# Optimization experiments

Hardware: AMD Instinct MI355X
Metric: run time of the kernel (lower is better)

The kernel has to match this reference:

```python
import jax, jax.numpy as jnp
import numpy as np

N_NODES = 50000
N_EDGES = 800000
EMBED_DIM = 256
HIDDEN_DIM = 128
OUT_DIM = 12
N_TARGETS = 4096


def gcn_conv(x, edge_index, W, b):
    """PyG-style GCNConv: add self-loops, symmetric deg^-1/2 normalization,
    linear transform then sparse aggregation."""
    n = x.shape[0]
    loop = jnp.arange(n)
    src = jnp.concatenate([edge_index[0], loop])
    dst = jnp.concatenate([edge_index[1], loop])
    # degree of destination nodes (incl. self loops)
    deg = jax.ops.segment_sum(jnp.ones_like(dst, dtype=x.dtype), dst, num_segments=n)
    dinv = jnp.where(deg > 0, jax.lax.rsqrt(deg), 0.0)
    norm = dinv[src] * dinv[dst]                     # [E+n]
    h = x @ W                                        # [n, out] transform first (PyG order)
    msgs = h[src] * norm[:, None]                    # [E+n, out]
    return jax.ops.segment_sum(msgs, dst, num_segments=n) + b


def setup_inputs() -> dict:
    key = jax.random.key(0)
    ks = jax.random.split(key, 9)
    x = jax.random.normal(ks[0], (N_NODES, EMBED_DIM), dtype=jnp.float32)
    edge_index = jax.random.randint(ks[1], (2, N_EDGES), 0, N_NODES, dtype=jnp.int64)
    target_mask = jax.random.randint(ks[2], (N_TARGETS,), 0, N_NODES, dtype=jnp.int64)
    s1 = 1.0 / np.sqrt(EMBED_DIM)
    s2 = 1.0 / np.sqrt(HIDDEN_DIM)
    W1 = jax.random.uniform(ks[3], (EMBED_DIM, HIDDEN_DIM), jnp.float32, -s1, s1)
    b1 = jnp.zeros((HIDDEN_DIM,), jnp.float32)
    W2 = jax.random.uniform(ks[4], (HIDDEN_DIM, HIDDEN_DIM), jnp.float32, -s2, s2)
    b2 = jnp.zeros((HIDDEN_DIM,), jnp.float32)
    Wr = jax.random.uniform(ks[5], (HIDDEN_DIM, OUT_DIM), jnp.float32, -s2, s2)
    br = jax.random.uniform(ks[6], (OUT_DIM,), jnp.float32, -s2, s2)
    return {"x": x, "edge_index": edge_index, "target_mask": target_mask,
            "W1": W1, "b1": b1, "W2": W2, "b2": b2, "Wr": Wr, "br": br}


def reference(x, edge_index, target_mask, W1, b1, W2, b2, Wr, br):
    h = jax.nn.relu(gcn_conv(x, edge_index, W1, b1))
    h = jax.nn.relu(gcn_conv(h, edge_index, W2, b2))
    pred = h[target_mask] @ Wr + br                  # [N_TARGETS, OUT_DIM]
    return pred
```

## Files before the change

### kernel.cpp

```cpp
#include <hip/hip_runtime.h>
#include <math.h>

#define N_NODES 50000
#define N_EDGES 800000
#define EMBED 256
#define HID 128
#define OUTD 12
#define N_TGT 4096

#define SCAN_NB 196
#define NPART 8
#define NODES_PER_PART 6250
#define RCAP 64
#define NB_G1 782

typedef short bf16x8 __attribute__((ext_vector_type(8)));
typedef float f32x4 __attribute__((ext_vector_type(4)));
typedef int intx4 __attribute__((ext_vector_type(4)));

__device__ __forceinline__ unsigned short f2b(float f) {
    union { float f; unsigned int u; } v;
    v.f = f;
    unsigned int u = v.u;
    return (unsigned short)((u + 0x7FFFu + ((u >> 16) & 1u)) >> 16);
}

__device__ __forceinline__ float b2f(unsigned short s) {
    union { unsigned int u; float f; } v;
    v.u = ((unsigned int)s) << 16;
    return v.f;
}

__global__ __launch_bounds__(256) void k_prelude(int* __restrict__ counts,
                                                 const float* __restrict__ W1,
                                                 unsigned short* __restrict__ Wt1,
                                                 const float* __restrict__ W2,
                                                 unsigned short* __restrict__ Wt2) {
    int i = blockIdx.x * 256 + threadIdx.x;
    if (i < N_NODES) counts[i] = 0;
    if (i < 32768) {
        int nn = i >> 8, k = i & 255;
        Wt1[nn * 256 + k] = f2b(W1[(size_t)k * 128 + nn]);
    } else if (i < 49152) {
        int j = i - 32768;
        int nn = j >> 7, k = j & 127;
        Wt2[nn * 128 + k] = f2b(W2[(size_t)k * 128 + nn]);
    }
}

template <int K, bool IS_BF16>
__device__ __forceinline__ void gemm_body(int gb, int tid, const void* __restrict__ Xv,
                                          const unsigned short* __restrict__ Wt,
                                          unsigned short* __restrict__ Hb, int n,
                                          unsigned short* As ) {
    const int row0 = gb * 64;
    const int w = tid >> 6, lane = tid & 63;
    const int lr = lane & 15, lg = lane >> 4;
    constexpr int NKS = K / 32;

    bf16x8 bfr[NKS][2];
#pragma unroll
    for (int ks = 0; ks < NKS; ++ks)
#pragma unroll
        for (int fn = 0; fn < 2; ++fn) {
            int colg = w * 32 + fn * 16 + lr;
            bfr[ks][fn] = *(const bf16x8*)&Wt[(size_t)colg * K + ks * 32 + lg * 8];
        }

    const int r0s = (tid * 2) >> 3, c0s = ((tid * 2) & 7) * 4;
    const int r1s = (tid * 2 + 1) >> 3, c1s = ((tid * 2 + 1) & 7) * 4;

    const float* Xf = (const float*)Xv;
    const unsigned short* Xb = (const unsigned short*)Xv;

    float4 f0 = make_float4(0.f, 0.f, 0.f, 0.f), f1 = f0;
    ushort4 u0 = make_ushort4(0, 0, 0, 0), u1 = u0;
    if (IS_BF16) {
        if (row0 + r0s < n) u0 = *(const ushort4*)&Xb[(size_t)(row0 + r0s) * K + c0s];
        if (row0 + r1s < n) u1 = *(const ushort4*)&Xb[(size_t)(row0 + r1s) * K + c1s];
    } else {
        if (row0 + r0s < n) f0 = *(const float4*)&Xf[(size_t)(row0 + r0s) * K + c0s];
        if (row0 + r1s < n) f1 = *(const float4*)&Xf[(size_t)(row0 + r1s) * K + c1s];
    }

    f32x4 acc[4][2] = {};
#pragma unroll
    for (int ks = 0; ks < NKS; ++ks) {
        __syncthreads();
        if (IS_BF16) {
            *(ushort4*)&As[r0s * 40 + c0s] = u0;
            *(ushort4*)&As[r1s * 40 + c1s] = u1;
        } else {
            *(ushort4*)&As[r0s * 40 + c0s] = make_ushort4(f2b(f0.x), f2b(f0.y), f2b(f0.z), f2b(f0.w));
            *(ushort4*)&As[r1s * 40 + c1s] = make_ushort4(f2b(f1.x), f2b(f1.y), f2b(f1.z), f2b(f1.w));
        }
        __syncthreads();
        if (ks + 1 < NKS) {
            int ko = (ks + 1) * 32;
            if (IS_BF16) {
                u0 = make_ushort4(0, 0, 0, 0); u1 = u0;
                if (row0 + r0s < n) u0 = *(const ushort4*)&Xb[(size_t)(row0 + r0s) * K + ko + c0s];
                if (row0 + r1s < n) u1 = *(const ushort4*)&Xb[(size_t)(row0 + r1s) * K + ko + c1s];
            } else {
                f0 = make_float4(0.f, 0.f, 0.f, 0.f); f1 = f0;
                if (row0 + r0s < n) f0 = *(const float4*)&Xf[(size_t)(row0 + r0s) * K + ko + c0s];
                if (row0 + r1s < n) f1 = *(const float4*)&Xf[(size_t)(row0 + r1s) * K + ko + c1s];
            }
        }
#pragma unroll
        for (int fm = 0; fm < 4; ++fm) {
            bf16x8 afr = *(const bf16x8*)&As[(fm * 16 + lr) * 40 + lg * 8];
#pragma unroll
            for (int fn = 0; fn < 2; ++fn)
                acc[fm][fn] = __builtin_amdgcn_mfma_f32_16x16x32_bf16(
                    afr, bfr[ks][fn], acc[fm][fn], 0, 0, 0);
        }
    }
#pragma unroll
    for (int fm = 0; fm < 4; ++fm) {
#pragma unroll
        for (int r = 0; r < 4; ++r) {
            int gr = row0 + fm * 16 + lg * 4 + r;
            if (gr < n) {
#pragma unroll
                for (int fn = 0; fn < 2; ++fn)
                    Hb[(size_t)gr * 128 + w * 32 + fn * 16 + lr] = f2b(acc[fm][fn][r]);
            }
        }
    }
}

__global__ __launch_bounds__(256) void k_fused1(const float* __restrict__ x,
                                                const unsigned short* __restrict__ Wt1,
                                                unsigned short* __restrict__ bufA,
                                                const int* __restrict__ src,
                                                const int* __restrict__ dst,
                                                int* __restrict__ counts,
                                                int* __restrict__ col_p, int nE4) {
    __shared__ unsigned short As[64 * 40];
    const int b = blockIdx.x, tid = threadIdx.x;
    if (b < NB_G1) {
        gemm_body<EMBED, false>(b, tid, x, Wt1, bufA, N_NODES, As);
        return;
    }
    int g = b & (NPART - 1);
    int i = ((b - NB_G1) >> 3) * 256 + tid;
    if (i >= nE4) return;
    intx4 d4 = *(const intx4*)&dst[i * 4];
    intx4 s4 = *(const intx4*)&src[i * 4];
#pragma unroll
    for (int q = 0; q < 4; ++q) {
        int d = d4[q];
        if ((unsigned)(d - g * NODES_PER_PART) < (unsigned)NODES_PER_PART) {
            int pos = atomicAdd(&counts[d], 1);
            if (pos < RCAP) col_p[d * RCAP + pos] = s4[q];
        }
    }
}

__global__ __launch_bounds__(256) void k_gemm2(const unsigned short* __restrict__ X,
                                               const unsigned short* __restrict__ Wt,
                                               unsigned short* __restrict__ Hb, int n) {
    __shared__ unsigned short As[64 * 40];
    gemm_body<HID, true>(blockIdx.x, threadIdx.x, X, Wt, Hb, n, As);
}

__global__ __launch_bounds__(256) void k_sort_dinv(const int* __restrict__ counts,
                                                   int* __restrict__ col_p,
                                                   float* __restrict__ dinv) {
    int wid = threadIdx.x >> 6;
    int lane = threadIdx.x & 63;
    int v = blockIdx.x * 4 + wid;
    if (v >= N_NODES) return;
    int cnt = counts[v];
    if (lane == 0) dinv[v] = rsqrtf(1.0f + (float)cnt);
    cnt = min(cnt, RCAP);
    if (cnt <= 1) return;
    int beg = v * RCAP;
    int key = (lane < cnt) ? col_p[beg + lane] : 0x7FFFFFFF;
#pragma unroll
    for (int k = 2; k <= 64; k <<= 1) {
#pragma unroll
        for (int j = k >> 1; j > 0; j >>= 1) {
            int other = __shfl_xor(key, j);
            bool up = ((lane & k) == 0);
            bool lower = ((lane & j) == 0);
            key = (lower == up) ? min(key, other) : max(key, other);
        }
    }
    if (lane < cnt) col_p[beg + lane] = key;
}

__device__ __forceinline__ f32x4 agg_core(const unsigned short* __restrict__ h,
                                          const int* __restrict__ counts,
                                          const int* __restrict__ col_p,
                                          const float* __restrict__ dinv,
                                          int v, int lane) {
    float dv = dinv[v];
    ushort4 hv = *(const ushort4*)&h[(size_t)v * HID + lane * 4];
    float sl = dv * dv;
    f32x4 a0 = {b2f(hv.x) * sl, b2f(hv.y) * sl, b2f(hv.z) * sl, b2f(hv.w) * sl};
    f32x4 a1 = {0.f, 0.f, 0.f, 0.f}, a2 = a1, a3 = a1;
    int beg = v * RCAP;
    int cnt = min(counts[v], RCAP);
    for (int j0 = 0; j0 < cnt; j0 += 32) {
        int m = cnt - j0; if (m > 32) m = 32;
        int sj = 0; float wj = 0.f;
        if (lane < m) {
            sj = col_p[beg + j0 + lane];
            wj = dinv[sj] * dv;
        }
        int M = (m + 3) & ~3;
        float w0 = __shfl(wj, 0, 32), w1 = __shfl(wj, 1, 32);
        float w2 = __shfl(wj, 2, 32), w3 = __shfl(wj, 3, 32);
        int s0 = __shfl(sj, 0, 32), s1 = __shfl(sj, 1, 32);
        int s2 = __shfl(sj, 2, 32), s3 = __shfl(sj, 3, 32);
        ushort4 q0 = *(const ushort4*)&h[(size_t)s0 * HID + lane * 4];
        ushort4 q1 = *(const ushort4*)&h[(size_t)s1 * HID + lane * 4];
        ushort4 q2 = *(const ushort4*)&h[(size_t)s2 * HID + lane * 4];
        ushort4 q3 = *(const ushort4*)&h[(size_t)s3 * HID + lane * 4];
        for (int jj = 0; jj < M; jj += 4) {
            ushort4 n0 = q0, n1 = q1, n2 = q2, n3 = q3;
            float nw0 = 0.f, nw1 = 0.f, nw2 = 0.f, nw3 = 0.f;
            if (jj + 4 < M) {
                int t0 = __shfl(sj, jj + 4, 32), t1 = __shfl(sj, jj + 5, 32);
                int t2 = __shfl(sj, jj + 6, 32), t3 = __shfl(sj, jj + 7, 32);
                nw0 = __shfl(wj, jj + 4, 32); nw1 = __shfl(wj, jj + 5, 32);
                nw2 = __shfl(wj, jj + 6, 32); nw3 = __shfl(wj, jj + 7, 32);
                n0 = *(const ushort4*)&h[(size_t)t0 * HID + lane * 4];
                n1 = *(const ushort4*)&h[(size_t)t1 * HID + lane * 4];
                n2 = *(const ushort4*)&h[(size_t)t2 * HID + lane * 4];
                n3 = *(const ushort4*)&h[(size_t)t3 * HID + lane * 4];
            }
            a0[0] = fmaf(b2f(q0.x), w0, a0[0]); a0[1] = fmaf(b2f(q0.y), w0, a0[1]);
            a0[2] = fmaf(b2f(q0.z), w0, a0[2]); a0[3] = fmaf(b2f(q0.w), w0, a0[3]);
            a1[0] = fmaf(b2f(q1.x), w1, a1[0]); a1[1] = fmaf(b2f(q1.y), w1, a1[1]);
            a1[2] = fmaf(b2f(q1.z), w1, a1[2]); a1[3] = fmaf(b2f(q1.w), w1, a1[3]);
            a2[0] = fmaf(b2f(q2.x), w2, a2[0]); a2[1] = fmaf(b2f(q2.y), w2, a2[1]);
            a2[2] = fmaf(b2f(q2.z), w2, a2[2]); a2[3] = fmaf(b2f(q2.w), w2, a2[3]);
            a3[0] = fmaf(b2f(q3.x), w3, a3[0]); a3[1] = fmaf(b2f(q3.y), w3, a3[1]);
            a3[2] = fmaf(b2f(q3.z), w3, a3[2]); a3[3] = fmaf(b2f(q3.w), w3, a3[3]);
            q0 = n0; q1 = n1; q2 = n2; q3 = n3;
            w0 = nw0; w1 = nw1; w2 = nw2; w3 = nw3;
        }
    }
    f32x4 r;
    r[0] = (a0[0] + a1[0]) + (a2[0] + a3[0]);
    r[1] = (a0[1] + a1[1]) + (a2[1] + a3[1]);
    r[2] = (a0[2] + a1[2]) + (a2[2] + a3[2]);
    r[3] = (a0[3] + a1[3]) + (a2[3] + a3[3]);
    return r;
}

__global__ __launch_bounds__(256) void k_agg_all(const unsigned short* __restrict__ h,
                                                 const int* __restrict__ counts,
                                                 const int* __restrict__ col_p,
                                                 const float* __restrict__ dinv,
                                                 const float* __restrict__ b,
                                                 unsigned short* __restrict__ out) {
    int t = blockIdx.x * 256 + threadIdx.x;
    int v = t >> 5;
    int lane = t & 31;
    if (v >= N_NODES) return;
    f32x4 a = agg_core(h, counts, col_p, dinv, v, lane);
    float4 bv = *(const float4*)&b[lane * 4];
    ushort4 r;
    r.x = f2b(fmaxf(a[0] + bv.x, 0.f));
    r.y = f2b(fmaxf(a[1] + bv.y, 0.f));
    r.z = f2b(fmaxf(a[2] + bv.z, 0.f));
    r.w = f2b(fmaxf(a[3] + bv.w, 0.f));
    *(ushort4*)&out[(size_t)v * HID + lane * 4] = r;
}

__global__ __launch_bounds__(256) void k_agg_tgt_final(const unsigned short* __restrict__ h,
                                                       const int* __restrict__ counts,
                                                       const int* __restrict__ col_p,
                                                       const float* __restrict__ dinv,
                                                       const int* __restrict__ tgt,
                                                       const float* __restrict__ b,
                                                       const float* __restrict__ Wr,
                                                       const float* __restrict__ br,
                                                       float* __restrict__ out) {
    int t = blockIdx.x * 256 + threadIdx.x;
    int tt = t >> 5;
    int lane = t & 31;
    if (tt >= N_TGT) return;
    int v = tgt[tt];
    f32x4 a = agg_core(h, counts, col_p, dinv, v, lane);
    float4 bv = *(const float4*)&b[lane * 4];
    float r0 = fmaxf(a[0] + bv.x, 0.f);
    float r1 = fmaxf(a[1] + bv.y, 0.f);
    float r2 = fmaxf(a[2] + bv.z, 0.f);
    float r3 = fmaxf(a[3] + bv.w, 0.f);
    const float* wr = &Wr[lane * 4 * OUTD];
#pragma unroll
    for (int j = 0; j < OUTD; ++j) {
        float p = r0 * wr[0 * OUTD + j] + r1 * wr[1 * OUTD + j] +
                  r2 * wr[2 * OUTD + j] + r3 * wr[3 * OUTD + j];
#pragma unroll
        for (int off = 16; off > 0; off >>= 1) p += __shfl_down(p, off, 32);
        if (lane == 0) out[tt * OUTD + j] = p + br[j];
    }
}

extern "C" void kernel_launch(void* const* d_in, const int* in_sizes, int n_in,
                              void* d_out, int out_size, void* d_ws, size_t ws_size,
                              hipStream_t stream) {
    const float* x  = (const float*)d_in[0];
    const int*   ei = (const int*)d_in[1];
    const int*   tm = (const int*)d_in[2];
    const float* W1 = (const float*)d_in[3];
    const float* b1 = (const float*)d_in[4];
    const float* W2 = (const float*)d_in[5];
    const float* b2 = (const float*)d_in[6];
    const float* Wr = (const float*)d_in[7];
    const float* br = (const float*)d_in[8];
    float* out = (float*)d_out;

    const int* e_src = ei;
    const int* e_dst = ei + N_EDGES;

    char* ws = (char*)d_ws;
    float*          dinv   = (float*)(ws + 0x000000);
    int*            counts = (int*)  (ws + 0x040000);
    unsigned short* Wt1    = (unsigned short*)(ws + 0x080000);
    unsigned short* Wt2    = (unsigned short*)(ws + 0x090000);
    int*            col_p  = (int*)  (ws + 0x200000);
    unsigned short* bufA   = (unsigned short*)(ws + 0xE40000);
    unsigned short* bufB   = (unsigned short*)(ws + 0x1B00000);

    const int NE4     = N_EDGES / 4;
    const int NB_FILL = ((NE4 + 255) / 256) * NPART;
    const int NB_F1   = NB_G1 + NB_FILL;
    const int NB_AGG  = (N_NODES * 32 + 255) / 256;
    const int NB_AGT  = (N_TGT * 32 + 255) / 256;
    const int NB_SORT = (N_NODES + 3) / 4;

    k_prelude<<<SCAN_NB, 256, 0, stream>>>(counts, W1, Wt1, W2, Wt2);
    k_fused1<<<NB_F1, 256, 0, stream>>>(x, Wt1, bufA, e_src, e_dst, counts, col_p, NE4);
    k_sort_dinv<<<NB_SORT, 256, 0, stream>>>(counts, col_p, dinv);

    k_agg_all<<<NB_AGG, 256, 0, stream>>>(bufA, counts, col_p, dinv, b1, bufB);

    k_gemm2<<<NB_G1, 256, 0, stream>>>(bufB, Wt2, bufA, N_NODES);
    k_agg_tgt_final<<<NB_AGT, 256, 0, stream>>>(bufA, counts, col_p, dinv, tm, b2, Wr, br, out);
}
```

Baseline: 135.8 us.

## Fuse neighbor sort and dinv into aggregation kernels, pad degree counters

Removes the separate sort/dinv kernel. Each aggregation block now bitonic-sorts its nodes' neighbor lists into LDS and computes deg^-1/2 on the fly from the counters. The per-node atomic counters are padded to a 64-byte stride so that atomics from different nodes do not contend on the same cache line. In exchange, the second aggregation sorts the rows again, the prelude writes 16x more zeroed memory, and reading neighbor counts now hits a strided layout instead of a dense dinv array.

```diff
diff --git a/kernel.cpp b/kernel.cpp
--- a/kernel.cpp
+++ b/kernel.cpp
@@ -13,6 +13,7 @@
 #define NODES_PER_PART 6250
 #define RCAP 64
 #define NB_G1 782
+#define CSTRIDE 16
 
 typedef short bf16x8 __attribute__((ext_vector_type(8)));
 typedef float f32x4 __attribute__((ext_vector_type(4)));
@@ -31,13 +32,17 @@
     return v.f;
 }
 
-__global__ __launch_bounds__(256) void k_prelude(int* __restrict__ counts,
+__global__ __launch_bounds__(256) void k_prelude(int* __restrict__ counts_p,
                                                  const float* __restrict__ W1,
                                                  unsigned short* __restrict__ Wt1,
                                                  const float* __restrict__ W2,
                                                  unsigned short* __restrict__ Wt2) {
     int i = blockIdx.x * 256 + threadIdx.x;
-    if (i < N_NODES) counts[i] = 0;
+    if (i < N_NODES) {
+        intx4 z = {0, 0, 0, 0};
+#pragma unroll
+        for (int q = 0; q < 4; ++q) *(intx4*)&counts_p[(size_t)i * CSTRIDE + q * 4] = z;
+    }
     if (i < 32768) {
         int nn = i >> 8, k = i & 255;
         Wt1[nn * 256 + k] = f2b(W1[(size_t)k * 128 + nn]);
@@ -135,7 +140,7 @@
                                                 unsigned short* __restrict__ bufA,
                                                 const int* __restrict__ src,
                                                 const int* __restrict__ dst,
-                                                int* __restrict__ counts,
+                                                int* __restrict__ counts_p,
                                                 int* __restrict__ col_p, int nE4) {
     __shared__ unsigned short As[64 * 40];
     const int b = blockIdx.x, tid = threadIdx.x;
@@ -152,7 +157,7 @@
     for (int q = 0; q < 4; ++q) {
         int d = d4[q];
         if ((unsigned)(d - g * NODES_PER_PART) < (unsigned)NODES_PER_PART) {
-            int pos = atomicAdd(&counts[d], 1);
+            int pos = atomicAdd(&counts_p[(size_t)d * CSTRIDE], 1);
             if (pos < RCAP) col_p[d * RCAP + pos] = s4[q];
         }
     }
@@ -165,50 +170,38 @@
     gemm_body<HID, true>(blockIdx.x, threadIdx.x, X, Wt, Hb, n, As);
 }
 
-__global__ __launch_bounds__(256) void k_sort_dinv(const int* __restrict__ counts,
-                                                   int* __restrict__ col_p,
-                                                   float* __restrict__ dinv) {
-    int wid = threadIdx.x >> 6;
-    int lane = threadIdx.x & 63;
-    int v = blockIdx.x * 4 + wid;
-    if (v >= N_NODES) return;
-    int cnt = counts[v];
-    if (lane == 0) dinv[v] = rsqrtf(1.0f + (float)cnt);
-    cnt = min(cnt, RCAP);
-    if (cnt <= 1) return;
-    int beg = v * RCAP;
-    int key = (lane < cnt) ? col_p[beg + lane] : 0x7FFFFFFF;
+__device__ __forceinline__ void sort_row_to_lds(const int* __restrict__ col_p,
+                                                int v, int cnt, int lane64,
+                                                int* __restrict__ srow) {
+    int key = 0x7FFFFFFF;
+    if (lane64 < cnt) key = col_p[v * RCAP + lane64];
 #pragma unroll
     for (int k = 2; k <= 64; k <<= 1) {
 #pragma unroll
         for (int j = k >> 1; j > 0; j >>= 1) {
             int other = __shfl_xor(key, j);
-            bool up = ((lane & k) == 0);
-            bool lower = ((lane & j) == 0);
+            bool up = ((lane64 & k) == 0);
+            bool lower = ((lane64 & j) == 0);
             key = (lower == up) ? min(key, other) : max(key, other);
         }
     }
-    if (lane < cnt) col_p[beg + lane] = key;
+    srow[lane64] = key;
 }
 
 __device__ __forceinline__ f32x4 agg_core(const unsigned short* __restrict__ h,
-                                          const int* __restrict__ counts,
-                                          const int* __restrict__ col_p,
-                                          const float* __restrict__ dinv,
-                                          int v, int lane) {
-    float dv = dinv[v];
+                                          const int* __restrict__ counts_p,
+                                          const int* __restrict__ srow,
+                                          int v, int cnt, int lane, float dv) {
     ushort4 hv = *(const ushort4*)&h[(size_t)v * HID + lane * 4];
     float sl = dv * dv;
     f32x4 a0 = {b2f(hv.x) * sl, b2f(hv.y) * sl, b2f(hv.z) * sl, b2f(hv.w) * sl};
     f32x4 a1 = {0.f, 0.f, 0.f, 0.f}, a2 = a1, a3 = a1;
-    int beg = v * RCAP;
-    int cnt = min(counts[v], RCAP);
     for (int j0 = 0; j0 < cnt; j0 += 32) {
         int m = cnt - j0; if (m > 32) m = 32;
         int sj = 0; float wj = 0.f;
         if (lane < m) {
-            sj = col_p[beg + j0 + lane];
-            wj = dinv[sj] * dv;
+            sj = srow[j0 + lane];
+            wj = rsqrtf(1.0f + (float)counts_p[(size_t)sj * CSTRIDE]) * dv;
         }
         int M = (m + 3) & ~3;
         float w0 = __shfl(wj, 0, 32), w1 = __shfl(wj, 1, 32);
@@ -253,16 +246,26 @@
 }
 
 __global__ __launch_bounds__(256) void k_agg_all(const unsigned short* __restrict__ h,
-                                                 const int* __restrict__ counts,
+                                                 const int* __restrict__ counts_p,
                                                  const int* __restrict__ col_p,
-                                                 const float* __restrict__ dinv,
                                                  const float* __restrict__ b,
                                                  unsigned short* __restrict__ out) {
-    int t = blockIdx.x * 256 + threadIdx.x;
-    int v = t >> 5;
-    int lane = t & 31;
-    if (v >= N_NODES) return;
-    f32x4 a = agg_core(h, counts, col_p, dinv, v, lane);
+    __shared__ int scol[8][64];
+    const int tid = threadIdx.x;
+    const int w = tid >> 6, lane64 = tid & 63;
+    const int base = blockIdx.x * 8;
+#pragma unroll
+    for (int s = 0; s < 2; ++s) {
+        int v = base + w * 2 + s;
+        int cnt = min(counts_p[(size_t)v * CSTRIDE], RCAP);
+        sort_row_to_lds(col_p, v, cnt, lane64, scol[w * 2 + s]);
+    }
+    __syncthreads();
+    const int hw = tid >> 5, lane = tid & 31;
+    const int v = base + hw;
+    int cnt = min(counts_p[(size_t)v * CSTRIDE], RCAP);
+    float dv = rsqrtf(1.0f + (float)counts_p[(size_t)v * CSTRIDE]);
+    f32x4 a = agg_core(h, counts_p, scol[hw], v, cnt, lane, dv);
     float4 bv = *(const float4*)&b[lane * 4];
     ushort4 r;
     r.x = f2b(fmaxf(a[0] + bv.x, 0.f));
@@ -273,20 +276,30 @@
 }
 
 __global__ __launch_bounds__(256) void k_agg_tgt_final(const unsigned short* __restrict__ h,
-                                                       const int* __restrict__ counts,
+                                                       const int* __restrict__ counts_p,
                                                        const int* __restrict__ col_p,
-                                                       const float* __restrict__ dinv,
                                                        const int* __restrict__ tgt,
                                                        const float* __restrict__ b,
                                                        const float* __restrict__ Wr,
                                                        const float* __restrict__ br,
                                                        float* __restrict__ out) {
-    int t = blockIdx.x * 256 + threadIdx.x;
-    int tt = t >> 5;
-    int lane = t & 31;
-    if (tt >= N_TGT) return;
-    int v = tgt[tt];
-    f32x4 a = agg_core(h, counts, col_p, dinv, v, lane);
+    __shared__ int scol[8][64];
+    const int tid = threadIdx.x;
+    const int w = tid >> 6, lane64 = tid & 63;
+    const int base = blockIdx.x * 8;
+#pragma unroll
+    for (int s = 0; s < 2; ++s) {
+        int v = tgt[base + w * 2 + s];
+        int cnt = min(counts_p[(size_t)v * CSTRIDE], RCAP);
+        sort_row_to_lds(col_p, v, cnt, lane64, scol[w * 2 + s]);
+    }
+    __syncthreads();
+    const int hw = tid >> 5, lane = tid & 31;
+    const int tt = base + hw;
+    const int v = tgt[tt];
+    int cnt = min(counts_p[(size_t)v * CSTRIDE], RCAP);
+    float dv = rsqrtf(1.0f + (float)counts_p[(size_t)v * CSTRIDE]);
+    f32x4 a = agg_core(h, counts_p, scol[hw], v, cnt, lane, dv);
     float4 bv = *(const float4*)&b[lane * 4];
     float r0 = fmaxf(a[0] + bv.x, 0.f);
     float r1 = fmaxf(a[1] + bv.y, 0.f);
@@ -321,27 +334,24 @@
     const int* e_dst = ei + N_EDGES;
 
     char* ws = (char*)d_ws;
-    float*          dinv   = (float*)(ws + 0x000000);
-    int*            counts = (int*)  (ws + 0x040000);
-    unsigned short* Wt1    = (unsigned short*)(ws + 0x080000);
-    unsigned short* Wt2    = (unsigned short*)(ws + 0x090000);
-    int*            col_p  = (int*)  (ws + 0x200000);
-    unsigned short* bufA   = (unsigned short*)(ws + 0xE40000);
-    unsigned short* bufB   = (unsigned short*)(ws + 0x1B00000);
+    int*            counts_p = (int*)  (ws + 0x040000);
+    unsigned short* Wt1      = (unsigned short*)(ws + 0x380000);
+    unsigned short* Wt2      = (unsigned short*)(ws + 0x390000);
+    int*            col_p    = (int*)  (ws + 0x400000);
+    unsigned short* bufA     = (unsigned short*)(ws + 0x1100000);
+    unsigned short* bufB     = (unsigned short*)(ws + 0x1E00000);
 
     const int NE4     = N_EDGES / 4;
     const int NB_FILL = ((NE4 + 255) / 256) * NPART;
     const int NB_F1   = NB_G1 + NB_FILL;
-    const int NB_AGG  = (N_NODES * 32 + 255) / 256;
-    const int NB_AGT  = (N_TGT * 32 + 255) / 256;
-    const int NB_SORT = (N_NODES + 3) / 4;
-
-    k_prelude<<<SCAN_NB, 256, 0, stream>>>(counts, W1, Wt1, W2, Wt2);
-    k_fused1<<<NB_F1, 256, 0, stream>>>(x, Wt1, bufA, e_src, e_dst, counts, col_p, NE4);
-    k_sort_dinv<<<NB_SORT, 256, 0, stream>>>(counts, col_p, dinv);
-
-    k_agg_all<<<NB_AGG, 256, 0, stream>>>(bufA, counts, col_p, dinv, b1, bufB);
+    const int NB_AGG  = N_NODES / 8;
+    const int NB_AGT  = N_TGT / 8;
+
+    k_prelude<<<SCAN_NB, 256, 0, stream>>>(counts_p, W1, Wt1, W2, Wt2);
+    k_fused1<<<NB_F1, 256, 0, stream>>>(x, Wt1, bufA, e_src, e_dst, counts_p, col_p, NE4);
+
+    k_agg_all<<<NB_AGG, 256, 0, stream>>>(bufA, counts_p, col_p, b1, bufB);
 
     k_gemm2<<<NB_G1, 256, 0, stream>>>(bufB, Wt2, bufA, N_NODES);
-    k_agg_tgt_final<<<NB_AGT, 256, 0, stream>>>(bufA, counts, col_p, dinv, tm, b2, Wr, br, out);
-}
+    k_agg_tgt_final<<<NB_AGT, 256, 0, stream>>>(bufA, counts_p, col_p, tm, b2, Wr, br, out);
+}
```

Result: no change. 135.8 us (-0.0%).
